# Kernel optimization log

Measured on AMD Instinct MI355X. Metric: run time of the kernel, lower is better.

The kernel has to match this reference:

```python
import jax, jax.numpy as jnp
import numpy as np

N_SPECIES = 4  # species ids 0..3


def setup_inputs() -> dict:
    key = jax.random.key(0)
    k1, k2, k3, k4 = jax.random.split(key, 4)
    NTA, O, NMAX = 65536, 512, 512
    rho = jax.random.normal(k1, (NTA, O), dtype=jnp.float32)
    # per-species expert Linear(O -> NMAX): weights stacked [S, O, NMAX], bias [S, NMAX]
    W = jax.random.normal(k2, (N_SPECIES, O, NMAX), dtype=jnp.float32) * (1.0 / np.sqrt(O))
    b = jax.random.normal(k3, (N_SPECIES, NMAX), dtype=jnp.float32) * 0.01
    symbols = jax.random.randint(k4, (NTA,), 0, N_SPECIES, dtype=jnp.int32)
    return {"rho": rho, "W": W, "b": b, "symbols": symbols}


def reference(rho, W, b, symbols):
    # Faithful to Gj.forward: coeff[mask] = expert_spe(rho[mask]) for each species.
    # Vectorized form: apply each species' Linear to all atoms (dense GEMM),
    # then select per-atom by species mask. Loop is over the small fixed
    # species set (4), not over data dims.
    NTA = rho.shape[0]
    nmax = W.shape[-1]
    coeff = jnp.zeros((NTA, nmax), dtype=rho.dtype)
    for spe in range(W.shape[0]):
        y = rho @ W[spe] + b[spe]            # [NTA, nmax]
        mask = (symbols == spe)[:, None]      # [NTA, 1]
        coeff = jnp.where(mask, y, coeff)
    return coeff
```

## Files before the change

### kernel.cpp

```cpp
#include <hip/hip_runtime.h>


#define NTA   65536
#define DIM_O 512
#define NMAXD 512
#define NSPE  4
#define BM    64
#define BK    64

typedef __attribute__((ext_vector_type(4))) float  f32x4;
typedef __attribute__((ext_vector_type(8))) short  bf16x8;

__device__ __forceinline__ short f2bf(float f) {
    unsigned u = __builtin_bit_cast(unsigned, f);
    u += 0x7FFFu + ((u >> 16) & 1u);
    return (short)(u >> 16);
}

__global__ void build_lists_kernel(const int* __restrict__ sym,
                                   int* __restrict__ counts,
                                   int* __restrict__ lists) {
    int i = blockIdx.x * 256 + threadIdx.x;
    int s = sym[i];
    int lane = threadIdx.x & 63;
    #pragma unroll
    for (int spe = 0; spe < NSPE; ++spe) {
        unsigned long long m = __ballot(s == spe);
        if (m == 0ull) continue;
        int leader = __ffsll(m) - 1;
        int base = 0;
        if (lane == leader) base = atomicAdd(&counts[spe], __popcll(m));
        base = __shfl(base, leader);
        if (s == spe) {
            int pos = __popcll(m & ((1ull << lane) - 1ull));
            lists[spe * NTA + base + pos] = i;
        }
    }
}

__global__ void pack_w_kernel(const float* __restrict__ W, short* __restrict__ Wp) {
    int idx = blockIdx.x * 256 + threadIdx.x;
    int j  = idx & 7;
    int l  = (idx >> 3) & 63;
    int nb = (idx >> 9) & 31;
    int kb = (idx >> 14) & 15;
    int s  = idx >> 18;
    int k = kb * 32 + (l >> 4) * 8 + j;
    int n = nb * 16 + (l & 15);
    Wp[idx] = f2bf(W[((size_t)s * DIM_O + k) * NMAXD + n]);
}

__global__ __launch_bounds__(256, 4)
void gemm_kernel(const float* __restrict__ rho,
                 const short* __restrict__ Wp,
                 const float* __restrict__ bias,
                 const int*  __restrict__ counts,
                 const int*  __restrict__ lists,
                 float* __restrict__ out)
{
    const int s   = blockIdx.x & 3;
    const int ch  = (blockIdx.x >> 2) & 1;
    const int mb  = blockIdx.x >> 3;
    const int cnt = counts[s];
    const int row0 = mb * BM;
    if (row0 >= cnt) return;
    int rows_here = cnt - row0; if (rows_here > BM) rows_here = BM;

    __shared__ int aidx[BM];
    __shared__ __align__(16) short Abuf[2][8 * 64 * 8];

    const int tid  = threadIdx.x;
    const int lane = tid & 63;
    const int w    = tid >> 6;
    const int lrow = lane & 15;
    const int lgr  = lane >> 4;

    if (tid < BM)
        aidx[tid] = lists[s * NTA + row0 + ((tid < rows_here) ? tid : 0)];
    __syncthreads();

    const float* gsrc = rho + (size_t)aidx[lane] * DIM_O + w * 16;
    const short* wbase = Wp + ((size_t)s * 512 + ch * 16 + w * 4) * 512 + lane * 8;

    f32x4 acc[4][4];
    #pragma unroll
    for (int m = 0; m < 4; ++m)
        #pragma unroll
        for (int n = 0; n < 4; ++n) acc[m][n] = (f32x4)0.0f;

    f32x4 st[4];
    { const f32x4* p = (const f32x4*)gsrc; st[0]=p[0]; st[1]=p[1]; st[2]=p[2]; st[3]=p[3]; }
    {
        short tmp[16];
        #pragma unroll
        for (int i = 0; i < 4; ++i)
            #pragma unroll
            for (int q = 0; q < 4; ++q) tmp[i*4+q] = f2bf(st[i][q]);
        *(bf16x8*)&Abuf[0][((2*w    )*64 + lane)*8] = *(const bf16x8*)&tmp[0];
        *(bf16x8*)&Abuf[0][((2*w + 1)*64 + lane)*8] = *(const bf16x8*)&tmp[8];
    }
    __syncthreads();

    for (int kt = 0; kt < 8; ++kt) {
        const int buf = kt & 1;
        if (kt < 7) {
            const f32x4* p = (const f32x4*)(gsrc + (kt + 1) * BK);
            st[0]=p[0]; st[1]=p[1]; st[2]=p[2]; st[3]=p[3];
        }
        #pragma unroll
        for (int ks = 0; ks < 2; ++ks) {
            const int kb = kt * 2 + ks;
            bf16x8 bfrag[4];
            #pragma unroll
            for (int nf = 0; nf < 4; ++nf)
                bfrag[nf] = *(const bf16x8*)(wbase + (size_t)(kb * 32 + nf) * 512);
            #pragma unroll
            for (int mf = 0; mf < 4; ++mf) {
                const bf16x8 afrag =
                    *(const bf16x8*)&Abuf[buf][((ks*4 + lgr)*64 + mf*16 + lrow)*8];
                #pragma unroll
                for (int nf = 0; nf < 4; ++nf)
                    acc[mf][nf] = __builtin_amdgcn_mfma_f32_16x16x32_bf16(
                        afrag, bfrag[nf], acc[mf][nf], 0, 0, 0);
            }
        }
        if (kt < 7) {
            short tmp[16];
            #pragma unroll
            for (int i = 0; i < 4; ++i)
                #pragma unroll
                for (int q = 0; q < 4; ++q) tmp[i*4+q] = f2bf(st[i][q]);
            short* base = Abuf[buf ^ 1];
            *(bf16x8*)&base[((2*w    )*64 + lane)*8] = *(const bf16x8*)&tmp[0];
            *(bf16x8*)&base[((2*w + 1)*64 + lane)*8] = *(const bf16x8*)&tmp[8];
            __syncthreads();
        }
    }

    float bv[4];
    #pragma unroll
    for (int nf = 0; nf < 4; ++nf)
        bv[nf] = bias[s * NMAXD + ch * 256 + w * 64 + nf * 16 + lrow];
    #pragma unroll
    for (int mf = 0; mf < 4; ++mf) {
        #pragma unroll
        for (int q = 0; q < 4; ++q) {
            const int r = mf * 16 + lgr * 4 + q;
            if (r < rows_here) {
                float* orow = out + (size_t)aidx[r] * NMAXD + ch * 256 + w * 64 + lrow;
                #pragma unroll
                for (int nf = 0; nf < 4; ++nf)
                    orow[nf * 16] = acc[mf][nf][q] + bv[nf];
            }
        }
    }
}

extern "C" void kernel_launch(void* const* d_in, const int* in_sizes, int n_in,
                              void* d_out, int out_size, void* d_ws, size_t ws_size,
                              hipStream_t stream) {
    const float* rho = (const float*)d_in[0];
    const float* W   = (const float*)d_in[1];
    const float* b   = (const float*)d_in[2];
    const int*   sym = (const int*)d_in[3];
    float* out = (float*)d_out;

    int*   counts = (int*)d_ws;
    int*   lists  = (int*)((char*)d_ws + 1024);
    short* Wp     = (short*)((char*)d_ws + 1024 + (size_t)NSPE * NTA * 4);

    hipMemsetAsync(counts, 0, NSPE * sizeof(int), stream);
    build_lists_kernel<<<NTA / 256, 256, 0, stream>>>(sym, counts, lists);
    pack_w_kernel<<<(NSPE * DIM_O * NMAXD) / 256, 256, 0, stream>>>(W, Wp);
    gemm_kernel<<<NSPE * 2 * (NTA / BM), 256, 0, stream>>>(rho, Wp, b, counts, lists, out);
}
```

Baseline: 148.9 us.

## Merge both column halves into one 512-thread block to halve A-tile gathers

Each block now covers all 512 output columns with 8 waves instead of two blocks each covering 256 columns. The gathered rho rows are therefore loaded from global memory and converted to bf16 only once per row tile, where before they were loaded twice. The staging load is also reorganised so that 8 threads share each row with 16-byte loads. Larger blocks may reduce occupancy and parallelism, and each block now synchronises more waves.

```diff
diff --git a/kernel.cpp b/kernel.cpp
--- a/kernel.cpp
+++ b/kernel.cpp
@@ -10,6 +10,7 @@
 
 typedef __attribute__((ext_vector_type(4))) float  f32x4;
 typedef __attribute__((ext_vector_type(8))) short  bf16x8;
+typedef __attribute__((ext_vector_type(4))) short  bf16x4;
 
 __device__ __forceinline__ short f2bf(float f) {
     unsigned u = __builtin_bit_cast(unsigned, f);
@@ -50,7 +51,7 @@
     Wp[idx] = f2bf(W[((size_t)s * DIM_O + k) * NMAXD + n]);
 }
 
-__global__ __launch_bounds__(256, 4)
+__global__ __launch_bounds__(512, 4)
 void gemm_kernel(const float* __restrict__ rho,
                  const short* __restrict__ Wp,
                  const float* __restrict__ bias,
@@ -59,8 +60,7 @@
                  float* __restrict__ out)
 {
     const int s   = blockIdx.x & 3;
-    const int ch  = (blockIdx.x >> 2) & 1;
-    const int mb  = blockIdx.x >> 3;
+    const int mb  = blockIdx.x >> 2;
     const int cnt = counts[s];
     const int row0 = mb * BM;
     if (row0 >= cnt) return;
@@ -79,8 +79,13 @@
         aidx[tid] = lists[s * NTA + row0 + ((tid < rows_here) ? tid : 0)];
     __syncthreads();
 
-    const float* gsrc = rho + (size_t)aidx[lane] * DIM_O + w * 16;
-    const short* wbase = Wp + ((size_t)s * 512 + ch * 16 + w * 4) * 512 + lane * 8;
+    const int srow  = tid >> 3;
+    const int scol8 = tid & 7;
+    const float* gsrc = rho + (size_t)aidx[srow] * DIM_O + scol8 * 4;
+    const int dso0 = (((scol8 >> 1)    ) * 64 + srow) * 8 + (scol8 & 1) * 4;
+    const int dso1 = (((scol8 >> 1) + 4) * 64 + srow) * 8 + (scol8 & 1) * 4;
+
+    const short* wbase = Wp + ((size_t)s * 512 + w * 4) * 512 + lane * 8;
 
     f32x4 acc[4][4];
     #pragma unroll
@@ -88,24 +93,23 @@
         #pragma unroll
         for (int n = 0; n < 4; ++n) acc[m][n] = (f32x4)0.0f;
 
-    f32x4 st[4];
-    { const f32x4* p = (const f32x4*)gsrc; st[0]=p[0]; st[1]=p[1]; st[2]=p[2]; st[3]=p[3]; }
+    f32x4 st0, st1;
+    st0 = *(const f32x4*)(gsrc);
+    st1 = *(const f32x4*)(gsrc + 32);
     {
-        short tmp[16];
+        bf16x4 a, b;
         #pragma unroll
-        for (int i = 0; i < 4; ++i)
-            #pragma unroll
-            for (int q = 0; q < 4; ++q) tmp[i*4+q] = f2bf(st[i][q]);
-        *(bf16x8*)&Abuf[0][((2*w    )*64 + lane)*8] = *(const bf16x8*)&tmp[0];
-        *(bf16x8*)&Abuf[0][((2*w + 1)*64 + lane)*8] = *(const bf16x8*)&tmp[8];
+        for (int q = 0; q < 4; ++q) { a[q] = f2bf(st0[q]); b[q] = f2bf(st1[q]); }
+        *(bf16x4*)&Abuf[0][dso0] = a;
+        *(bf16x4*)&Abuf[0][dso1] = b;
     }
     __syncthreads();
 
     for (int kt = 0; kt < 8; ++kt) {
         const int buf = kt & 1;
         if (kt < 7) {
-            const f32x4* p = (const f32x4*)(gsrc + (kt + 1) * BK);
-            st[0]=p[0]; st[1]=p[1]; st[2]=p[2]; st[3]=p[3];
+            st0 = *(const f32x4*)(gsrc + (kt + 1) * BK);
+            st1 = *(const f32x4*)(gsrc + (kt + 1) * BK + 32);
         }
         #pragma unroll
         for (int ks = 0; ks < 2; ++ks) {
@@ -117,7 +121,7 @@
             #pragma unroll
             for (int mf = 0; mf < 4; ++mf) {
                 const bf16x8 afrag =
-                    *(const bf16x8*)&Abuf[buf][((ks*4 + lgr)*64 + mf*16 + lrow)*8];
+                    *(const bf16x8*)&Abuf[buf][((ks * 4 + lgr) * 64 + mf * 16 + lrow) * 8];
                 #pragma unroll
                 for (int nf = 0; nf < 4; ++nf)
                     acc[mf][nf] = __builtin_amdgcn_mfma_f32_16x16x32_bf16(
@@ -125,14 +129,12 @@
             }
         }
         if (kt < 7) {
-            short tmp[16];
+            bf16x4 a, b;
             #pragma unroll
-            for (int i = 0; i < 4; ++i)
-                #pragma unroll
-                for (int q = 0; q < 4; ++q) tmp[i*4+q] = f2bf(st[i][q]);
+            for (int q = 0; q < 4; ++q) { a[q] = f2bf(st0[q]); b[q] = f2bf(st1[q]); }
             short* base = Abuf[buf ^ 1];
-            *(bf16x8*)&base[((2*w    )*64 + lane)*8] = *(const bf16x8*)&tmp[0];
-            *(bf16x8*)&base[((2*w + 1)*64 + lane)*8] = *(const bf16x8*)&tmp[8];
+            *(bf16x4*)&base[dso0] = a;
+            *(bf16x4*)&base[dso1] = b;
             __syncthreads();
         }
     }
@@ -140,14 +142,14 @@
     float bv[4];
     #pragma unroll
     for (int nf = 0; nf < 4; ++nf)
-        bv[nf] = bias[s * NMAXD + ch * 256 + w * 64 + nf * 16 + lrow];
+        bv[nf] = bias[s * NMAXD + w * 64 + nf * 16 + lrow];
     #pragma unroll
     for (int mf = 0; mf < 4; ++mf) {
         #pragma unroll
         for (int q = 0; q < 4; ++q) {
             const int r = mf * 16 + lgr * 4 + q;
             if (r < rows_here) {
-                float* orow = out + (size_t)aidx[r] * NMAXD + ch * 256 + w * 64 + lrow;
+                float* orow = out + (size_t)aidx[r] * NMAXD + w * 64 + lrow;
                 #pragma unroll
                 for (int nf = 0; nf < 4; ++nf)
                     orow[nf * 16] = acc[mf][nf][q] + bv[nf];
@@ -172,5 +174,5 @@
     hipMemsetAsync(counts, 0, NSPE * sizeof(int), stream);
     build_lists_kernel<<<NTA / 256, 256, 0, stream>>>(sym, counts, lists);
     pack_w_kernel<<<(NSPE * DIM_O * NMAXD) / 256, 256, 0, stream>>>(W, Wp);
-    gemm_kernel<<<NSPE * 2 * (NTA / BM), 256, 0, stream>>>(rho, Wp, b, counts, lists, out);
+    gemm_kernel<<<NSPE * (NTA / BM), 512, 0, stream>>>(rho, Wp, b, counts, lists, out);
 }
```

Measured after the change: 132.2 us. 11.2% less time.

## Group atoms by species within each 64-row tile instead of global lists

Applied to the files above, without the earlier changes.

Drops the global species list build (memset, ballot/atomic kernel) and instead has each block take 64 contiguous atoms, bucket them by species in shared memory into 16-row MFMA fragments (up to 7 padded fragments), and compute each fragment against its species' weights over all 512 output columns. rho reads become contiguous and the per-block A tile is loaded once for the full N width, removing the duplicated A loads of the two column halves and two small launches. In exchange, padding fragments waste MFMA work (about 5 to 7 fragments instead of 4), B loads are issued per fragment, and a swizzled LDS layout plus larger blocks raise register pressure.

```diff
diff --git a/kernel.cpp b/kernel.cpp
--- a/kernel.cpp
+++ b/kernel.cpp
@@ -5,7 +5,7 @@
 #define DIM_O 512
 #define NMAXD 512
 #define NSPE  4
-#define BM    64
+#define NSLOT 112
 #define BK    64
 
 typedef __attribute__((ext_vector_type(4))) float  f32x4;
@@ -15,27 +15,6 @@
     unsigned u = __builtin_bit_cast(unsigned, f);
     u += 0x7FFFu + ((u >> 16) & 1u);
     return (short)(u >> 16);
-}
-
-__global__ void build_lists_kernel(const int* __restrict__ sym,
-                                   int* __restrict__ counts,
-                                   int* __restrict__ lists) {
-    int i = blockIdx.x * 256 + threadIdx.x;
-    int s = sym[i];
-    int lane = threadIdx.x & 63;
-    #pragma unroll
-    for (int spe = 0; spe < NSPE; ++spe) {
-        unsigned long long m = __ballot(s == spe);
-        if (m == 0ull) continue;
-        int leader = __ffsll(m) - 1;
-        int base = 0;
-        if (lane == leader) base = atomicAdd(&counts[spe], __popcll(m));
-        base = __shfl(base, leader);
-        if (s == spe) {
-            int pos = __popcll(m & ((1ull << lane) - 1ull));
-            lists[spe * NTA + base + pos] = i;
-        }
-    }
 }
 
 __global__ void pack_w_kernel(const float* __restrict__ W, short* __restrict__ Wp) {
@@ -50,107 +29,129 @@
     Wp[idx] = f2bf(W[((size_t)s * DIM_O + k) * NMAXD + n]);
 }
 
-__global__ __launch_bounds__(256, 4)
+__global__ __launch_bounds__(512, 2)
 void gemm_kernel(const float* __restrict__ rho,
                  const short* __restrict__ Wp,
                  const float* __restrict__ bias,
-                 const int*  __restrict__ counts,
-                 const int*  __restrict__ lists,
+                 const int*  __restrict__ sym,
                  float* __restrict__ out)
 {
-    const int s   = blockIdx.x & 3;
-    const int ch  = (blockIdx.x >> 2) & 1;
-    const int mb  = blockIdx.x >> 3;
-    const int cnt = counts[s];
-    const int row0 = mb * BM;
-    if (row0 >= cnt) return;
-    int rows_here = cnt - row0; if (rows_here > BM) rows_here = BM;
-
-    __shared__ int aidx[BM];
-    __shared__ __align__(16) short Abuf[2][8 * 64 * 8];
-
+    const int g    = blockIdx.x;
     const int tid  = threadIdx.x;
     const int lane = tid & 63;
     const int w    = tid >> 6;
     const int lrow = lane & 15;
     const int lgr  = lane >> 4;
 
-    if (tid < BM)
-        aidx[tid] = lists[s * NTA + row0 + ((tid < rows_here) ? tid : 0)];
+    __shared__ int slotOf[64];
+    __shared__ int s2a[NSLOT];
+    __shared__ int fspe[8];
+    __shared__ int nfrag_sh;
+    __shared__ __align__(16) short Ab[2][NSLOT * 8 * 8];
+
+    if (tid < NSLOT) s2a[tid] = -1;
+    if (tid < 64) {
+        const int s = sym[g * 64 + tid];
+        const unsigned long long m0 = __ballot(s == 0);
+        const unsigned long long m1 = __ballot(s == 1);
+        const unsigned long long m2 = __ballot(s == 2);
+        const unsigned long long m3 = __ballot(s == 3);
+        const int F1 = (__popcll(m0) + 15) >> 4;
+        const int F2 = F1 + (int)((__popcll(m1) + 15) >> 4);
+        const int F3 = F2 + (int)((__popcll(m2) + 15) >> 4);
+        const int F4 = F3 + (int)((__popcll(m3) + 15) >> 4);
+        const unsigned long long ms = (s == 0) ? m0 : (s == 1) ? m1 : (s == 2) ? m2 : m3;
+        const int Fs = (s == 0) ? 0 : (s == 1) ? F1 : (s == 2) ? F2 : F3;
+        const unsigned long long below = (1ull << tid) - 1ull;
+        const int slot = Fs * 16 + (int)__popcll(ms & below);
+        slotOf[tid] = slot;
+        s2a[slot] = tid;
+        if (tid < F4) fspe[tid] = (tid >= F1) + (tid >= F2) + (tid >= F3);
+        if (tid == 0) nfrag_sh = F4;
+    }
     __syncthreads();
 
-    const float* gsrc = rho + (size_t)aidx[lane] * DIM_O + w * 16;
-    const short* wbase = Wp + ((size_t)s * 512 + ch * 16 + w * 4) * 512 + lane * 8;
+    const int nfrag = nfrag_sh;
+    int sfr[7];
+    #pragma unroll
+    for (int f = 0; f < 7; ++f) sfr[f] = (f < nfrag) ? fspe[f] : 0;
 
-    f32x4 acc[4][4];
-    #pragma unroll
-    for (int m = 0; m < 4; ++m)
+    const int c      = tid & 7;
+    const int nrow   = tid >> 3;
+    const int myslot = slotOf[nrow];
+    const int wa16   = c * NSLOT + (myslot ^ c);
+    const float* gsrc = rho + ((size_t)(g * 64 + nrow)) * DIM_O + c * 8;
+
+    f32x4 v0, v1;
+    v0 = *(const f32x4*)(gsrc);
+    v1 = *(const f32x4*)(gsrc + 4);
+    {
+        bf16x8 pk;
         #pragma unroll
-        for (int n = 0; n < 4; ++n) acc[m][n] = (f32x4)0.0f;
-
-    f32x4 st[4];
-    { const f32x4* p = (const f32x4*)gsrc; st[0]=p[0]; st[1]=p[1]; st[2]=p[2]; st[3]=p[3]; }
-    {
-        short tmp[16];
-        #pragma unroll
-        for (int i = 0; i < 4; ++i)
-            #pragma unroll
-            for (int q = 0; q < 4; ++q) tmp[i*4+q] = f2bf(st[i][q]);
-        *(bf16x8*)&Abuf[0][((2*w    )*64 + lane)*8] = *(const bf16x8*)&tmp[0];
-        *(bf16x8*)&Abuf[0][((2*w + 1)*64 + lane)*8] = *(const bf16x8*)&tmp[8];
+        for (int q = 0; q < 4; ++q) { pk[q] = f2bf(v0[q]); pk[4 + q] = f2bf(v1[q]); }
+        *(bf16x8*)&Ab[0][wa16 * 8] = pk;
     }
     __syncthreads();
+
+    f32x4 acc[7][4];
+    #pragma unroll
+    for (int f = 0; f < 7; ++f)
+        #pragma unroll
+        for (int n = 0; n < 4; ++n) acc[f][n] = (f32x4)0.0f;
 
     for (int kt = 0; kt < 8; ++kt) {
         const int buf = kt & 1;
         if (kt < 7) {
-            const f32x4* p = (const f32x4*)(gsrc + (kt + 1) * BK);
-            st[0]=p[0]; st[1]=p[1]; st[2]=p[2]; st[3]=p[3];
+            v0 = *(const f32x4*)(gsrc + (kt + 1) * BK);
+            v1 = *(const f32x4*)(gsrc + (kt + 1) * BK + 4);
         }
         #pragma unroll
         for (int ks = 0; ks < 2; ++ks) {
-            const int kb = kt * 2 + ks;
-            bf16x8 bfrag[4];
+            const int cA = ks * 4 + lgr;
             #pragma unroll
-            for (int nf = 0; nf < 4; ++nf)
-                bfrag[nf] = *(const bf16x8*)(wbase + (size_t)(kb * 32 + nf) * 512);
-            #pragma unroll
-            for (int mf = 0; mf < 4; ++mf) {
-                const bf16x8 afrag =
-                    *(const bf16x8*)&Abuf[buf][((ks*4 + lgr)*64 + mf*16 + lrow)*8];
-                #pragma unroll
-                for (int nf = 0; nf < 4; ++nf)
-                    acc[mf][nf] = __builtin_amdgcn_mfma_f32_16x16x32_bf16(
-                        afrag, bfrag[nf], acc[mf][nf], 0, 0, 0);
+            for (int f = 0; f < 7; ++f) {
+                if (f < nfrag) {
+                    const short* wb = Wp + ((size_t)sfr[f] * 512 + w * 4) * 512 + lane * 8;
+                    bf16x8 bfr[4];
+                    #pragma unroll
+                    for (int nf = 0; nf < 4; ++nf)
+                        bfr[nf] = *(const bf16x8*)
+                            (wb + (size_t)((kt * 2 + ks) * 32 + nf) * 512);
+                    const bf16x8 af =
+                        *(const bf16x8*)&Ab[buf][(cA * NSLOT + ((16 * f + lrow) ^ cA)) * 8];
+                    #pragma unroll
+                    for (int nf = 0; nf < 4; ++nf)
+                        acc[f][nf] = __builtin_amdgcn_mfma_f32_16x16x32_bf16(
+                            af, bfr[nf], acc[f][nf], 0, 0, 0);
+                }
             }
         }
         if (kt < 7) {
-            short tmp[16];
+            bf16x8 pk;
             #pragma unroll
-            for (int i = 0; i < 4; ++i)
-                #pragma unroll
-                for (int q = 0; q < 4; ++q) tmp[i*4+q] = f2bf(st[i][q]);
-            short* base = Abuf[buf ^ 1];
-            *(bf16x8*)&base[((2*w    )*64 + lane)*8] = *(const bf16x8*)&tmp[0];
-            *(bf16x8*)&base[((2*w + 1)*64 + lane)*8] = *(const bf16x8*)&tmp[8];
+            for (int q = 0; q < 4; ++q) { pk[q] = f2bf(v0[q]); pk[4 + q] = f2bf(v1[q]); }
+            *(bf16x8*)&Ab[buf ^ 1][wa16 * 8] = pk;
             __syncthreads();
         }
     }
 
-    float bv[4];
     #pragma unroll
-    for (int nf = 0; nf < 4; ++nf)
-        bv[nf] = bias[s * NMAXD + ch * 256 + w * 64 + nf * 16 + lrow];
-    #pragma unroll
-    for (int mf = 0; mf < 4; ++mf) {
-        #pragma unroll
-        for (int q = 0; q < 4; ++q) {
-            const int r = mf * 16 + lgr * 4 + q;
-            if (r < rows_here) {
-                float* orow = out + (size_t)aidx[r] * NMAXD + ch * 256 + w * 64 + lrow;
-                #pragma unroll
-                for (int nf = 0; nf < 4; ++nf)
-                    orow[nf * 16] = acc[mf][nf][q] + bv[nf];
+    for (int f = 0; f < 7; ++f) {
+        if (f < nfrag) {
+            const int sp = sfr[f];
+            float bv[4];
+            #pragma unroll
+            for (int nf = 0; nf < 4; ++nf)
+                bv[nf] = bias[sp * NMAXD + w * 64 + nf * 16 + lrow];
+            #pragma unroll
+            for (int q = 0; q < 4; ++q) {
+                const int atom = s2a[16 * f + lgr * 4 + q];
+                if (atom >= 0) {
+                    float* orow = out + ((size_t)(g * 64 + atom)) * NMAXD + w * 64 + lrow;
+                    #pragma unroll
+                    for (int nf = 0; nf < 4; ++nf)
+                        orow[nf * 16] = acc[f][nf][q] + bv[nf];
+                }
             }
         }
     }
@@ -165,12 +166,8 @@
     const int*   sym = (const int*)d_in[3];
     float* out = (float*)d_out;
 
-    int*   counts = (int*)d_ws;
-    int*   lists  = (int*)((char*)d_ws + 1024);
-    short* Wp     = (short*)((char*)d_ws + 1024 + (size_t)NSPE * NTA * 4);
+    short* Wp = (short*)d_ws;
 
-    hipMemsetAsync(counts, 0, NSPE * sizeof(int), stream);
-    build_lists_kernel<<<NTA / 256, 256, 0, stream>>>(sym, counts, lists);
     pack_w_kernel<<<(NSPE * DIM_O * NMAXD) / 256, 256, 0, stream>>>(W, Wp);
-    gemm_kernel<<<NSPE * 2 * (NTA / BM), 256, 0, stream>>>(rho, Wp, b, counts, lists, out);
+    gemm_kernel<<<NTA / 64, 512, 0, stream>>>(rho, Wp, b, sym, out);
 }
```

New measurement: 208.2 us. 1.4x slower.
